# Kernel optimization log

Hardware: AMD Instinct MI355X
Metric: run time of the kernel (lower is better)

Reference implementation:

```python
import jax, jax.numpy as jnp
import numpy as np

D_MODEL = 1024
D_KEY = 64
N_HEADS = 16
B, T = 4, 2048


def setup_inputs() -> dict:
    key = jax.random.key(0)
    ks = jax.random.split(key, 12)
    s = 0.02
    return {
        "keys": jax.random.normal(ks[0], (B, T, D_MODEL), jnp.float32),
        "queries": jax.random.normal(ks[1], (B, T, D_MODEL), jnp.float32),
        "values": jax.random.normal(ks[2], (B, T, D_MODEL), jnp.float32),
        "pad_mask": jnp.ones((B, T), jnp.int32),
        "WK_w": jax.random.normal(ks[3], (D_KEY * N_HEADS, D_MODEL), jnp.float32) * s,
        "WK_b": jnp.zeros((D_KEY * N_HEADS,), jnp.float32),
        "WQ_w": jax.random.normal(ks[4], (D_KEY * N_HEADS, D_MODEL), jnp.float32) * s,
        "WQ_b": jnp.zeros((D_KEY * N_HEADS,), jnp.float32),
        "WV_w": jax.random.normal(ks[5], (D_KEY * N_HEADS, D_MODEL), jnp.float32) * s,
        "WV_b": jnp.zeros((D_KEY * N_HEADS,), jnp.float32),
        "WO_w": jax.random.normal(ks[6], (D_MODEL, D_KEY * N_HEADS), jnp.float32) * s,
        "WO_b": jnp.zeros((D_MODEL,), jnp.float32),
    }


def reference(keys, queries, values, pad_mask, WK_w, WK_b, WQ_w, WQ_b, WV_w, WV_b, WO_w, WO_b):
    # NOTE: the original torch module calls masked_fill (non-inplace) and discards
    # the result, so neither the causal mask nor pad_mask has any effect. We
    # faithfully reproduce that: no masking. pad_mask is an unused constant.
    batch, time = keys.shape[:2]
    k = keys @ WK_w.T + WK_b      # [B,T,H*dk]
    q = queries @ WQ_w.T + WQ_b
    v = values @ WV_w.T + WV_b

    def split_heads(x):
        return x.reshape(batch, time, N_HEADS, D_KEY).transpose(0, 2, 1, 3)  # [B,H,T,dk]

    k, q, v = split_heads(k), split_heads(q), split_heads(v)
    # scores[t,s] = k_t . q_s / sqrt(d_key)  (K and Q swapped, as in source)
    scores = jnp.einsum("bhtd,bhsd->bhts", k, q) / jnp.sqrt(jnp.float32(D_KEY))
    attn = jax.nn.softmax(scores, axis=-1)             # [B,H,T,T]
    ctx = jnp.einsum("bhts,bhsd->bhtd", attn, v)       # [B,H,T,dk]
    ctx = ctx.transpose(0, 2, 1, 3).reshape(batch, time, N_HEADS * D_KEY)
    return ctx @ WO_w.T + WO_b
```

## Files before the change

kernel.cpp:

```cpp
#include <hip/hip_runtime.h>

typedef unsigned short u16;
typedef unsigned int u32;
typedef __attribute__((ext_vector_type(8))) short short8;
typedef __attribute__((ext_vector_type(4))) float f32x4;

__device__ __forceinline__ u16 f2bf(float f) {
    unsigned int u = __float_as_uint(f);
    u += 0x7fffu + ((u >> 16) & 1u);
    return (u16)(u >> 16);
}

__device__ __forceinline__ u32 pack_trunc(float a, float b) {
    return __builtin_amdgcn_perm(__float_as_uint(b), __float_as_uint(a), 0x07060302u);
}

__device__ __forceinline__ void gload16(const u16* g, const u16* l) {
    __builtin_amdgcn_global_load_lds(
        (const __attribute__((address_space(1))) unsigned int*)g,
        (__attribute__((address_space(3))) unsigned int*)l, 16, 0, 0);
}

__global__ __launch_bounds__(256) void cast_all(const float* __restrict__ k,
                                                const float* __restrict__ q,
                                                const float* __restrict__ v,
                                                const float* __restrict__ wk,
                                                const float* __restrict__ wq,
                                                const float* __restrict__ wv,
                                                const float* __restrict__ wo,
                                                u16* __restrict__ Xk, u16* __restrict__ Xq,
                                                u16* __restrict__ Xv, u16* __restrict__ Wk,
                                                u16* __restrict__ Wq, u16* __restrict__ Wv,
                                                u16* __restrict__ Wo) {
    size_t i = ((size_t)blockIdx.x * 256 + threadIdx.x) * 8;
    const float* src; u16* dst; size_t off;
    if (i < 25165824) {
        int r = (int)(i >> 23); off = i & 8388607;
        src = r == 0 ? k : (r == 1 ? q : v);
        dst = r == 0 ? Xk : (r == 1 ? Xq : Xv);
    } else {
        size_t j = i - 25165824;
        int r = (int)(j >> 20); off = j & 1048575;
        src = r == 0 ? wk : (r == 1 ? wq : (r == 2 ? wv : wo));
        dst = r == 0 ? Wk : (r == 1 ? Wq : (r == 2 ? Wv : Wo));
    }
    float4 a = *(const float4*)(src + off);
    float4 b = *(const float4*)(src + off + 4);
    union { u16 h[8]; uint4 u; } r8;
    r8.h[0] = f2bf(a.x); r8.h[1] = f2bf(a.y); r8.h[2] = f2bf(a.z); r8.h[3] = f2bf(a.w);
    r8.h[4] = f2bf(b.x); r8.h[5] = f2bf(b.y); r8.h[6] = f2bf(b.z); r8.h[7] = f2bf(b.w);
    *(uint4*)(dst + off) = r8.u;
}


__device__ __forceinline__ void stage_tile(const u16* __restrict__ X, const u16* __restrict__ W,
                                           int i0, int j0, int kt, u16* sA, u16* sB,
                                           int tid, int wave) {
    const int r = tid >> 3;
    const int sg = (tid & 7) ^ (r & 7);
    const u16* gA = X + (size_t)(i0 + r) * 1024 + kt + sg * 8;
    const u16* gB = W + (size_t)(j0 + r) * 1024 + kt + sg * 8;
    const u16* dA = sA + wave * 512;
    const u16* dB = sB + wave * 512;
    gload16(gA,               dA);
    gload16(gA + 64 * 1024,   dA + 4096);
    gload16(gA + 128 * 1024,  dA + 8192);
    gload16(gA + 192 * 1024,  dA + 12288);
    gload16(gB,               dB);
    gload16(gB + 64 * 1024,   dB + 4096);
}

__device__ __forceinline__ void tile_mfma(const u16* sA, const u16* sB,
                                          f32x4 (&acc)[8][2],
                                          int wm, int wn, int quad, int l16) {
    const int sx = l16 & 7;
    short8 bf[2][2];
    #pragma unroll
    for (int nf = 0; nf < 2; nf++)
        #pragma unroll
        for (int kh = 0; kh < 2; kh++) {
            int row = wn * 32 + nf * 16 + l16;
            int slot = (quad + kh * 4) ^ sx;
            bf[nf][kh] = *(const short8*)&sB[row * 64 + slot * 8];
        }
    #pragma unroll
    for (int mh = 0; mh < 2; mh++) {
        short8 af[4][2];
        #pragma unroll
        for (int mf = 0; mf < 4; mf++)
            #pragma unroll
            for (int kh = 0; kh < 2; kh++) {
                int row = wm * 128 + mh * 64 + mf * 16 + l16;
                int slot = (quad + kh * 4) ^ sx;
                af[mf][kh] = *(const short8*)&sA[row * 64 + slot * 8];
            }
        #pragma unroll
        for (int mf = 0; mf < 4; mf++)
            #pragma unroll
            for (int nf = 0; nf < 2; nf++)
                #pragma unroll
                for (int kh = 0; kh < 2; kh++)
                    acc[mh * 4 + mf][nf] = __builtin_amdgcn_mfma_f32_16x16x32_bf16(
                        af[mf][kh], bf[nf][kh], acc[mh * 4 + mf][nf], 0, 0, 0);
    }
}

#define GEMM_PIPELINE(X, W)                                                              \
    stage_tile(X, W, i0, j0, 0,  sAr,         sBr,        tid, wave);                    \
    stage_tile(X, W, i0, j0, 64, sAr + 16384, sBr + 8192, tid, wave);                    \
    int rs = 0;                                                                          \
    _Pragma("unroll 1")                                                                  \
    for (int t = 0; t < 14; t++) {                                                       \
        asm volatile("s_waitcnt vmcnt(6)" ::: "memory");                                 \
        __builtin_amdgcn_s_barrier();                                                    \
        __builtin_amdgcn_s_setprio(1);                                                   \
        tile_mfma(sAr + rs * 16384, sBr + rs * 8192, acc, wm, wn, quad, l16);            \
        __builtin_amdgcn_s_setprio(0);                                                   \
        __builtin_amdgcn_s_barrier();                                                    \
        int ss = rs + 2; if (ss >= 3) ss -= 3;                                           \
        stage_tile(X, W, i0, j0, (t + 2) * 64, sAr + ss * 16384, sBr + ss * 8192,        \
                   tid, wave);                                                           \
        rs = (rs == 2) ? 0 : rs + 1;                                                     \
    }                                                                                    \
    asm volatile("s_waitcnt vmcnt(6)" ::: "memory");             \
    __builtin_amdgcn_s_barrier();                                                        \
    tile_mfma(sAr + rs * 16384, sBr + rs * 8192, acc, wm, wn, quad, l16);                \
    __builtin_amdgcn_s_barrier();                                                        \
    rs = (rs == 2) ? 0 : rs + 1;                                                         \
    asm volatile("s_waitcnt vmcnt(0)" ::: "memory");                     \
    __builtin_amdgcn_s_barrier();                                                        \
    tile_mfma(sAr + rs * 16384, sBr + rs * 8192, acc, wm, wn, quad, l16);

__global__ __launch_bounds__(512, 2) void gemm_qkv(const u16* __restrict__ Xk,
                                                   const u16* __restrict__ Xq,
                                                   const u16* __restrict__ Xv,
                                                   const u16* __restrict__ Wk,
                                                   const u16* __restrict__ Wq,
                                                   const u16* __restrict__ Wv,
                                                   const float* __restrict__ bK,
                                                   const float* __restrict__ bQ,
                                                   const float* __restrict__ bV,
                                                   u16* __restrict__ Kbh,
                                                   u16* __restrict__ Qbh,
                                                   u16* __restrict__ Vtg,
                                                   float kscale) {
    extern __shared__ __align__(16) u16 smem[];
    u16* sAr = smem;
    u16* sBr = smem + 49152;
    const int f  = blockIdx.x;
    const int wg = (f & 7) * 96 + (f >> 3);
    const int z  = wg >> 8;
    const int r8 = wg & 255;
    const int i0 = (r8 >> 3) * 256;
    const int j0 = (r8 & 7) * 128;

    const u16* X = z == 0 ? Xk : (z == 1 ? Xq : Xv);
    const u16* W = z == 0 ? Wk : (z == 1 ? Wq : Wv);
    const float* bias = z == 0 ? bK : (z == 1 ? bQ : bV);
    u16* out = z == 0 ? Kbh : (z == 1 ? Qbh : Vtg);
    const float scale = z == 0 ? kscale : 1.0f;

    const int tid  = threadIdx.x;
    const int wave = tid >> 6, lane = tid & 63;
    const int quad = lane >> 4, l16 = lane & 15;
    const int wm = wave >> 2, wn = wave & 3;

    f32x4 acc[8][2];
    #pragma unroll
    for (int m = 0; m < 8; m++) {
        acc[m][0] = (f32x4){0.f, 0.f, 0.f, 0.f};
        acc[m][1] = (f32x4){0.f, 0.f, 0.f, 0.f};
    }

    GEMM_PIPELINE(X, W)

    #pragma unroll
    for (int m = 0; m < 8; m++) {
        #pragma unroll
        for (int nf = 0; nf < 2; nf++) {
            int j = j0 + wn * 32 + nf * 16 + l16;
            float bj = bias[j];
            #pragma unroll
            for (int r = 0; r < 4; r++) {
                int i = i0 + wm * 128 + m * 16 + quad * 4 + r;
                float v = (acc[m][nf][r] + bj) * scale;
                int b = i >> 11, tt = i & 2047;
                int h = j >> 6,  dd = j & 63;
                size_t idx;
                if (z == 2) idx = (((size_t)(b * 16 + h)) * 64 + dd) * 2048 + tt;
                else        idx = (((size_t)(b * 16 + h)) * 2048 + tt) * 64 + dd;
                out[idx] = f2bf(v);
            }
        }
    }
}

__global__ __launch_bounds__(512, 2) void gemm_out(const u16* __restrict__ X,
                                                   const u16* __restrict__ W,
                                                   const float* __restrict__ bias,
                                                   float* __restrict__ out) {
    extern __shared__ __align__(16) u16 smem[];
    u16* sAr = smem;
    u16* sBr = smem + 49152;
    const int f  = blockIdx.x;
    const int wg = (f & 7) * 32 + (f >> 3);
    const int i0 = (wg >> 3) * 256;
    const int j0 = (wg & 7) * 128;

    const int tid  = threadIdx.x;
    const int wave = tid >> 6, lane = tid & 63;
    const int quad = lane >> 4, l16 = lane & 15;
    const int wm = wave >> 2, wn = wave & 3;

    f32x4 acc[8][2];
    #pragma unroll
    for (int m = 0; m < 8; m++) {
        acc[m][0] = (f32x4){0.f, 0.f, 0.f, 0.f};
        acc[m][1] = (f32x4){0.f, 0.f, 0.f, 0.f};
    }

    GEMM_PIPELINE(X, W)

    #pragma unroll
    for (int m = 0; m < 8; m++) {
        #pragma unroll
        for (int nf = 0; nf < 2; nf++) {
            int j = j0 + wn * 32 + nf * 16 + l16;
            float bj = bias[j];
            #pragma unroll
            for (int r = 0; r < 4; r++) {
                int i = i0 + wm * 128 + m * 16 + quad * 4 + r;
                out[(size_t)i * 1024 + j] = acc[m][nf][r] + bj;
            }
        }
    }
}

#define QST 72

__global__ __launch_bounds__(256, 2) void attn_kernel(const u16* __restrict__ Kbh,
                                                      const u16* __restrict__ Qbh,
                                                      const u16* __restrict__ Vtg,
                                                      u16* __restrict__ ctx) {
    __shared__ u16 sQ[64 * QST];
    __shared__ u16 sVt[64 * QST];
    __shared__ u16 sP[4 * 2 * 16 * QST];
    const int f = blockIdx.x;
    const int bh = (f & 7) | ((f >> 6) << 3);
    const int tx = (f >> 3) & 7;
    const int tid  = threadIdx.x;
    const int wave = tid >> 6, lane = tid & 63;
    const int quad = lane >> 4, l16 = lane & 15;
    const int t0 = tx * 256;
    const int tw = t0 + wave * 64;
    const size_t base = (size_t)bh * 2048 * 64;

    short8 bk[4][2];
    #pragma unroll
    for (int g = 0; g < 4; g++) {
        const u16* kr = Kbh + base + (size_t)(tw + g * 16 + l16) * 64 + quad * 8;
        bk[g][0] = *(const short8*)kr;
        bk[g][1] = *(const short8*)(kr + 32);
    }
    const short8 ones = {0x3F80, 0x3F80, 0x3F80, 0x3F80, 0x3F80, 0x3F80, 0x3F80, 0x3F80};

    f32x4 accO[4][4];
    #pragma unroll
    for (int g = 0; g < 4; g++)
        #pragma unroll
        for (int dt = 0; dt < 4; dt++) accO[g][dt] = (f32x4){0.f, 0.f, 0.f, 0.f};
    f32x4 accL[4];
    #pragma unroll
    for (int g = 0; g < 4; g++) accL[g] = (f32x4){0.f, 0.f, 0.f, 0.f};

    const int srow = tid >> 2, seg = tid & 3;
    u16* sPw = sP + wave * 2 * 16 * QST;

    for (int s0 = 0; s0 < 2048; s0 += 64) {
        __syncthreads();
        {
            const uint4* gq = (const uint4*)(Qbh + base + (size_t)(s0 + srow) * 64 + seg * 16);
            uint4 q0 = gq[0], q1 = gq[1];
            *(uint4*)&sQ[srow * QST + seg * 16]     = q0;
            *(uint4*)&sQ[srow * QST + seg * 16 + 8] = q1;
        }
        {
            const uint4* gv = (const uint4*)(Vtg + ((size_t)bh * 64 + srow) * 2048 + s0 + seg * 16);
            uint4 v0 = gv[0], v1 = gv[1];
            *(uint4*)&sVt[srow * QST + seg * 16]     = v0;
            *(uint4*)&sVt[srow * QST + seg * 16 + 8] = v1;
        }
        __syncthreads();

        short8 aq[4][2], av[2][4];
        #pragma unroll
        for (int nt = 0; nt < 4; nt++) {
            aq[nt][0] = *(const short8*)&sQ[(nt * 16 + l16) * QST + quad * 8];
            aq[nt][1] = *(const short8*)&sQ[(nt * 16 + l16) * QST + 32 + quad * 8];
        }
        #pragma unroll
        for (int kk = 0; kk < 2; kk++)
            #pragma unroll
            for (int dt = 0; dt < 4; dt++)
                av[kk][dt] = *(const short8*)&sVt[(dt * 16 + l16) * QST + kk * 32 + quad * 8];

        #pragma unroll
        for (int g = 0; g < 4; g++) {
            f32x4 aS[4];
            #pragma unroll
            for (int nt = 0; nt < 4; nt++) {
                f32x4 s = __builtin_amdgcn_mfma_f32_16x16x32_bf16(aq[nt][0], bk[g][0],
                            (f32x4){0.f, 0.f, 0.f, 0.f}, 0, 0, 0);
                aS[nt] = __builtin_amdgcn_mfma_f32_16x16x32_bf16(aq[nt][1], bk[g][1], s, 0, 0, 0);
            }
            u16* pb = sPw + (g & 1) * 16 * QST;
            #pragma unroll
            for (int nt = 0; nt < 4; nt++) {
                float p0 = __builtin_amdgcn_exp2f(aS[nt][0]);
                float p1 = __builtin_amdgcn_exp2f(aS[nt][1]);
                float p2 = __builtin_amdgcn_exp2f(aS[nt][2]);
                float p3 = __builtin_amdgcn_exp2f(aS[nt][3]);
                uint2 pk = { pack_trunc(p0, p1), pack_trunc(p2, p3) };
                *(uint2*)&pb[l16 * QST + nt * 16 + quad * 4] = pk;
            }
            #pragma unroll
            for (int kk = 0; kk < 2; kk++) {
                short8 bp = *(const short8*)&pb[l16 * QST + kk * 32 + quad * 8];
                accL[g] = __builtin_amdgcn_mfma_f32_16x16x32_bf16(ones, bp, accL[g], 0, 0, 0);
                #pragma unroll
                for (int dt = 0; dt < 4; dt++)
                    accO[g][dt] = __builtin_amdgcn_mfma_f32_16x16x32_bf16(av[kk][dt], bp, accO[g][dt], 0, 0, 0);
            }
        }
    }

    const int b = bh >> 4, h = bh & 15;
    #pragma unroll
    for (int g = 0; g < 4; g++) {
        float inv = 1.f / accL[g][0];
        int t = tw + g * 16 + l16;
        u16* orow = ctx + ((size_t)(b * 2048 + t)) * 1024 + h * 64;
        #pragma unroll
        for (int dt = 0; dt < 4; dt++) {
            union { u16 h4[4]; uint2 u; } o;
            #pragma unroll
            for (int r = 0; r < 4; r++) o.h4[r] = f2bf(accO[g][dt][r] * inv);
            *(uint2*)&orow[dt * 16 + quad * 4] = o.u;
        }
    }
}

extern "C" void kernel_launch(void* const* d_in, const int* in_sizes, int n_in,
                              void* d_out, int out_size, void* d_ws, size_t ws_size,
                              hipStream_t stream) {
    const float* keys    = (const float*)d_in[0];
    const float* queries = (const float*)d_in[1];
    const float* values  = (const float*)d_in[2];
    const float* WKb = (const float*)d_in[5];
    const float* WQb = (const float*)d_in[7];
    const float* WVb = (const float*)d_in[9];
    const float* WOb = (const float*)d_in[11];

    char* ws = (char*)d_ws;
    const size_t MB = 1 << 20;
    u16* Kbh = (u16*)(ws + 0 * MB);
    u16* Qbh = (u16*)(ws + 16 * MB);
    u16* Vtg = (u16*)(ws + 32 * MB);
    u16* Xk  = (u16*)(ws + 48 * MB);
    u16* Xq  = (u16*)(ws + 64 * MB);
    u16* Xv  = (u16*)(ws + 80 * MB);
    u16* Wk  = (u16*)(ws + 96 * MB);
    u16* Wq  = (u16*)(ws + 98 * MB);
    u16* Wv  = (u16*)(ws + 100 * MB);
    u16* Wo  = (u16*)(ws + 102 * MB);
    u16* ctx = (u16*)(ws + 48 * MB);

    static bool attr_done = false;
    if (!attr_done) {
        hipFuncSetAttribute((const void*)gemm_qkv,
                            hipFuncAttributeMaxDynamicSharedMemorySize, 147456);
        hipFuncSetAttribute((const void*)gemm_out,
                            hipFuncAttributeMaxDynamicSharedMemorySize, 147456);
        attr_done = true;
    }

    cast_all<<<14336, 256, 0, stream>>>(keys, queries, values,
                                        (const float*)d_in[4], (const float*)d_in[6],
                                        (const float*)d_in[8], (const float*)d_in[10],
                                        Xk, Xq, Xv, Wk, Wq, Wv, Wo);

    const float kscale = 1.4426950408889634f * 0.125f;
    gemm_qkv<<<768, 512, 147456, stream>>>(Xk, Xq, Xv, Wk, Wq, Wv,
                                           WKb, WQb, WVb, Kbh, Qbh, Vtg, kscale);

    attn_kernel<<<512, 256, 0, stream>>>(Kbh, Qbh, Vtg, ctx);

    gemm_out<<<256, 512, 147456, stream>>>(ctx, Wo, WOb, (float*)d_out);
}
```

Baseline: 358.3 us.

## Switch projection GEMMs to 256x256 tiles with a double-buffered phased pipeline

```diff
diff --git a/kernel.cpp b/kernel.cpp
--- a/kernel.cpp
+++ b/kernel.cpp
@@ -53,83 +53,84 @@
 }
 
 
-__device__ __forceinline__ void stage_tile(const u16* __restrict__ X, const u16* __restrict__ W,
-                                           int i0, int j0, int kt, u16* sA, u16* sB,
-                                           int tid, int wave) {
-    const int r = tid >> 3;
-    const int sg = (tid & 7) ^ (r & 7);
-    const u16* gA = X + (size_t)(i0 + r) * 1024 + kt + sg * 8;
-    const u16* gB = W + (size_t)(j0 + r) * 1024 + kt + sg * 8;
-    const u16* dA = sA + wave * 512;
-    const u16* dB = sB + wave * 512;
-    gload16(gA,               dA);
-    gload16(gA + 64 * 1024,   dA + 4096);
-    gload16(gA + 128 * 1024,  dA + 8192);
-    gload16(gA + 192 * 1024,  dA + 12288);
-    gload16(gB,               dB);
-    gload16(gB + 64 * 1024,   dB + 4096);
-}
-
-__device__ __forceinline__ void tile_mfma(const u16* sA, const u16* sB,
-                                          f32x4 (&acc)[8][2],
-                                          int wm, int wn, int quad, int l16) {
-    const int sx = l16 & 7;
-    short8 bf[2][2];
-    #pragma unroll
-    for (int nf = 0; nf < 2; nf++)
-        #pragma unroll
-        for (int kh = 0; kh < 2; kh++) {
-            int row = wn * 32 + nf * 16 + l16;
-            int slot = (quad + kh * 4) ^ sx;
-            bf[nf][kh] = *(const short8*)&sB[row * 64 + slot * 8];
-        }
-    #pragma unroll
-    for (int mh = 0; mh < 2; mh++) {
-        short8 af[4][2];
-        #pragma unroll
-        for (int mf = 0; mf < 4; mf++)
-            #pragma unroll
-            for (int kh = 0; kh < 2; kh++) {
-                int row = wm * 128 + mh * 64 + mf * 16 + l16;
-                int slot = (quad + kh * 4) ^ sx;
-                af[mf][kh] = *(const short8*)&sA[row * 64 + slot * 8];
-            }
-        #pragma unroll
-        for (int mf = 0; mf < 4; mf++)
-            #pragma unroll
-            for (int nf = 0; nf < 2; nf++)
-                #pragma unroll
-                for (int kh = 0; kh < 2; kh++)
-                    acc[mh * 4 + mf][nf] = __builtin_amdgcn_mfma_f32_16x16x32_bf16(
-                        af[mf][kh], bf[nf][kh], acc[mh * 4 + mf][nf], 0, 0, 0);
-    }
-}
-
-#define GEMM_PIPELINE(X, W)                                                              \
-    stage_tile(X, W, i0, j0, 0,  sAr,         sBr,        tid, wave);                    \
-    stage_tile(X, W, i0, j0, 64, sAr + 16384, sBr + 8192, tid, wave);                    \
-    int rs = 0;                                                                          \
-    _Pragma("unroll 1")                                                                  \
-    for (int t = 0; t < 14; t++) {                                                       \
-        asm volatile("s_waitcnt vmcnt(6)" ::: "memory");                                 \
-        __builtin_amdgcn_s_barrier();                                                    \
-        __builtin_amdgcn_s_setprio(1);                                                   \
-        tile_mfma(sAr + rs * 16384, sBr + rs * 8192, acc, wm, wn, quad, l16);            \
-        __builtin_amdgcn_s_setprio(0);                                                   \
-        __builtin_amdgcn_s_barrier();                                                    \
-        int ss = rs + 2; if (ss >= 3) ss -= 3;                                           \
-        stage_tile(X, W, i0, j0, (t + 2) * 64, sAr + ss * 16384, sBr + ss * 8192,        \
-                   tid, wave);                                                           \
-        rs = (rs == 2) ? 0 : rs + 1;                                                     \
-    }                                                                                    \
-    asm volatile("s_waitcnt vmcnt(6)" ::: "memory");             \
-    __builtin_amdgcn_s_barrier();                                                        \
-    tile_mfma(sAr + rs * 16384, sBr + rs * 8192, acc, wm, wn, quad, l16);                \
-    __builtin_amdgcn_s_barrier();                                                        \
-    rs = (rs == 2) ? 0 : rs + 1;                                                         \
-    asm volatile("s_waitcnt vmcnt(0)" ::: "memory");                     \
-    __builtin_amdgcn_s_barrier();                                                        \
-    tile_mfma(sAr + rs * 16384, sBr + rs * 8192, acc, wm, wn, quad, l16);
+#define RD_A(bufp, mh, mf, kh) \
+  (*(const short8*)((bufp) + wm * 8192 + ((mh) * 64 + (mf) * 16 + l16) * 64 + \
+                    ((((kh) * 4 + quad)) ^ swz) * 8))
+#define RD_B(bufp, nh, nf, kh) \
+  (*(const short8*)((bufp) + (wn >> 1) * 8192 + \
+                    ((wn & 1) * 64 + (nh) * 32 + (nf) * 16 + l16) * 64 + \
+                    ((((kh) * 4 + quad)) ^ swz) * 8))
+
+#define STAGE_A(bufn, kt) { \
+    u16* d = sAr + (bufn) * 16384 + tid * 8; \
+    const u16* g = gA + (kt); \
+    gload16(g,          d); \
+    gload16(g + 65536,  d + 4096); \
+    gload16(g + 131072, d + 8192); \
+    gload16(g + 196608, d + 12288); }
+
+#define STAGE_B(bufn, kt) { \
+    u16* d = sBr + (bufn) * 16384 + tid * 8; \
+    const u16* g = gB + (kt); \
+    gload16(g,          d); \
+    gload16(g + 65536,  d + 4096); \
+    gload16(g + 131072, d + 8192); \
+    gload16(g + 196608, d + 12288); }
+
+#define MFMA_Q(mh, nh, A, B) \
+  _Pragma("unroll") for (int mf = 0; mf < 4; mf++) \
+  _Pragma("unroll") for (int nf = 0; nf < 2; nf++) \
+  _Pragma("unroll") for (int kh = 0; kh < 2; kh++) \
+    acc[(mh) * 4 + mf][(nh) * 2 + nf] = __builtin_amdgcn_mfma_f32_16x16x32_bf16( \
+        A[mf][kh], B[nf][kh], acc[(mh) * 4 + mf][(nh) * 2 + nf], 0, 0, 0);
+
+#define PHASE_SYNC() \
+    __builtin_amdgcn_s_barrier(); \
+    asm volatile("s_waitcnt lgkmcnt(0)" ::: "memory"); \
+    __builtin_amdgcn_sched_barrier(0);
+
+#define GEMM256_PIPELINE(X_, W_) \
+  const int sRow = tid >> 3; \
+  const int sColSw = ((tid & 7) ^ (sRow & 7)) * 8; \
+  const u16* gA = (X_) + (size_t)(i0 + sRow) * 1024 + sColSw; \
+  const u16* gB = (W_) + (size_t)(j0 + sRow) * 1024 + sColSw; \
+  const int swz = l16 & 7; \
+  STAGE_A(0, 0); STAGE_B(0, 0); \
+  asm volatile("s_waitcnt vmcnt(0)" ::: "memory"); \
+  __builtin_amdgcn_s_barrier(); \
+  _Pragma("unroll 1") \
+  for (int t = 0; t < 16; t++) { \
+    const int bc = t & 1; const int bn = bc ^ 1; const int ktn = (t + 1) * 64; \
+    const u16* bufA = sAr + bc * 16384; \
+    const u16* bufB = sBr + bc * 16384; \
+    short8 a[4][2], b0[2][2], b1[2][2]; \
+     \
+    _Pragma("unroll") for (int mf = 0; mf < 4; mf++) \
+      _Pragma("unroll") for (int kh = 0; kh < 2; kh++) a[mf][kh] = RD_A(bufA, 0, mf, kh); \
+    _Pragma("unroll") for (int nf = 0; nf < 2; nf++) \
+      _Pragma("unroll") for (int kh = 0; kh < 2; kh++) b0[nf][kh] = RD_B(bufB, 0, nf, kh); \
+    if (t < 15) { STAGE_A(bn, ktn); } \
+    PHASE_SYNC(); \
+    __builtin_amdgcn_s_setprio(1); MFMA_Q(0, 0, a, b0); __builtin_amdgcn_s_setprio(0); \
+    __builtin_amdgcn_s_barrier(); \
+     \
+    _Pragma("unroll") for (int nf = 0; nf < 2; nf++) \
+      _Pragma("unroll") for (int kh = 0; kh < 2; kh++) b1[nf][kh] = RD_B(bufB, 1, nf, kh); \
+    if (t < 15) { STAGE_B(bn, ktn); } \
+    PHASE_SYNC(); \
+    __builtin_amdgcn_s_setprio(1); MFMA_Q(0, 1, a, b1); __builtin_amdgcn_s_setprio(0); \
+    __builtin_amdgcn_s_barrier(); \
+     \
+    _Pragma("unroll") for (int mf = 0; mf < 4; mf++) \
+      _Pragma("unroll") for (int kh = 0; kh < 2; kh++) a[mf][kh] = RD_A(bufA, 1, mf, kh); \
+    PHASE_SYNC(); \
+    __builtin_amdgcn_s_setprio(1); MFMA_Q(1, 1, a, b1); __builtin_amdgcn_s_setprio(0); \
+    __builtin_amdgcn_s_barrier(); \
+     \
+    __builtin_amdgcn_s_setprio(1); MFMA_Q(1, 0, a, b0); __builtin_amdgcn_s_setprio(0); \
+    asm volatile("s_waitcnt vmcnt(0)" ::: "memory"); \
+    __builtin_amdgcn_s_barrier(); \
+  }
 
 __global__ __launch_bounds__(512, 2) void gemm_qkv(const u16* __restrict__ Xk,
                                                    const u16* __restrict__ Xq,
@@ -146,13 +147,13 @@
                                                    float kscale) {
     extern __shared__ __align__(16) u16 smem[];
     u16* sAr = smem;
-    u16* sBr = smem + 49152;
+    u16* sBr = smem + 32768;
     const int f  = blockIdx.x;
-    const int wg = (f & 7) * 96 + (f >> 3);
-    const int z  = wg >> 8;
-    const int r8 = wg & 255;
-    const int i0 = (r8 >> 3) * 256;
-    const int j0 = (r8 & 7) * 128;
+    const int wg = (f & 7) * 48 + (f >> 3);
+    const int z  = wg >> 7;
+    const int r7 = wg & 127;
+    const int i0 = (r7 >> 2) * 256;
+    const int j0 = (r7 & 3) * 256;
 
     const u16* X = z == 0 ? Xk : (z == 1 ? Xq : Xv);
     const u16* W = z == 0 ? Wk : (z == 1 ? Wq : Wv);
@@ -165,25 +166,24 @@
     const int quad = lane >> 4, l16 = lane & 15;
     const int wm = wave >> 2, wn = wave & 3;
 
-    f32x4 acc[8][2];
+    f32x4 acc[8][4];
+    #pragma unroll
+    for (int m = 0; m < 8; m++)
+        #pragma unroll
+        for (int n = 0; n < 4; n++) acc[m][n] = (f32x4){0.f, 0.f, 0.f, 0.f};
+
+    GEMM256_PIPELINE(X, W)
+
     #pragma unroll
     for (int m = 0; m < 8; m++) {
-        acc[m][0] = (f32x4){0.f, 0.f, 0.f, 0.f};
-        acc[m][1] = (f32x4){0.f, 0.f, 0.f, 0.f};
-    }
-
-    GEMM_PIPELINE(X, W)
-
-    #pragma unroll
-    for (int m = 0; m < 8; m++) {
-        #pragma unroll
-        for (int nf = 0; nf < 2; nf++) {
-            int j = j0 + wn * 32 + nf * 16 + l16;
+        #pragma unroll
+        for (int n = 0; n < 4; n++) {
+            int j = j0 + wn * 64 + n * 16 + l16;
             float bj = bias[j];
             #pragma unroll
             for (int r = 0; r < 4; r++) {
                 int i = i0 + wm * 128 + m * 16 + quad * 4 + r;
-                float v = (acc[m][nf][r] + bj) * scale;
+                float v = (acc[m][n][r] + bj) * scale;
                 int b = i >> 11, tt = i & 2047;
                 int h = j >> 6,  dd = j & 63;
                 size_t idx;
@@ -201,36 +201,35 @@
                                                    float* __restrict__ out) {
     extern __shared__ __align__(16) u16 smem[];
     u16* sAr = smem;
-    u16* sBr = smem + 49152;
+    u16* sBr = smem + 32768;
     const int f  = blockIdx.x;
-    const int wg = (f & 7) * 32 + (f >> 3);
-    const int i0 = (wg >> 3) * 256;
-    const int j0 = (wg & 7) * 128;
+    const int wg = (f & 7) * 16 + (f >> 3);
+    const int i0 = (wg >> 2) * 256;
+    const int j0 = (wg & 3) * 256;
 
     const int tid  = threadIdx.x;
     const int wave = tid >> 6, lane = tid & 63;
     const int quad = lane >> 4, l16 = lane & 15;
     const int wm = wave >> 2, wn = wave & 3;
 
-    f32x4 acc[8][2];
+    f32x4 acc[8][4];
+    #pragma unroll
+    for (int m = 0; m < 8; m++)
+        #pragma unroll
+        for (int n = 0; n < 4; n++) acc[m][n] = (f32x4){0.f, 0.f, 0.f, 0.f};
+
+    GEMM256_PIPELINE(X, W)
+
     #pragma unroll
     for (int m = 0; m < 8; m++) {
-        acc[m][0] = (f32x4){0.f, 0.f, 0.f, 0.f};
-        acc[m][1] = (f32x4){0.f, 0.f, 0.f, 0.f};
-    }
-
-    GEMM_PIPELINE(X, W)
-
-    #pragma unroll
-    for (int m = 0; m < 8; m++) {
-        #pragma unroll
-        for (int nf = 0; nf < 2; nf++) {
-            int j = j0 + wn * 32 + nf * 16 + l16;
+        #pragma unroll
+        for (int n = 0; n < 4; n++) {
+            int j = j0 + wn * 64 + n * 16 + l16;
             float bj = bias[j];
             #pragma unroll
             for (int r = 0; r < 4; r++) {
                 int i = i0 + wm * 128 + m * 16 + quad * 4 + r;
-                out[(size_t)i * 1024 + j] = acc[m][nf][r] + bj;
+                out[(size_t)i * 1024 + j] = acc[m][n][r] + bj;
             }
         }
     }
@@ -378,9 +377,9 @@
     static bool attr_done = false;
     if (!attr_done) {
         hipFuncSetAttribute((const void*)gemm_qkv,
-                            hipFuncAttributeMaxDynamicSharedMemorySize, 147456);
+                            hipFuncAttributeMaxDynamicSharedMemorySize, 131072);
         hipFuncSetAttribute((const void*)gemm_out,
-                            hipFuncAttributeMaxDynamicSharedMemorySize, 147456);
+                            hipFuncAttributeMaxDynamicSharedMemorySize, 131072);
         attr_done = true;
     }
 
@@ -390,10 +389,10 @@
                                         Xk, Xq, Xv, Wk, Wq, Wv, Wo);
 
     const float kscale = 1.4426950408889634f * 0.125f;
-    gemm_qkv<<<768, 512, 147456, stream>>>(Xk, Xq, Xv, Wk, Wq, Wv,
+    gemm_qkv<<<384, 512, 131072, stream>>>(Xk, Xq, Xv, Wk, Wq, Wv,
                                            WKb, WQb, WVb, Kbh, Qbh, Vtg, kscale);
 
     attn_kernel<<<512, 256, 0, stream>>>(Kbh, Qbh, Vtg, ctx);
 
-    gemm_out<<<256, 512, 147456, stream>>>(ctx, Wo, WOb, (float*)d_out);
-}
+    gemm_out<<<128, 512, 131072, stream>>>(ctx, Wo, WOb, (float*)d_out);
+}
```

Result: slower. 381.0 us (+6.3%).
